# Performance work log

Measured on AMD Instinct MI355X. Metric: run time of the kernel, lower is better.

## Reference

```python
import jax, jax.numpy as jnp
import numpy as np

B, T, C = 2, 2048, 2048
H = 16
HD = C // H  # 128; kv_size == hidden_size so kv head dim == HD


def setup_inputs() -> dict:
    key = jax.random.key(0)
    ks = jax.random.split(key, 5)
    s = 0.02
    return {
        "x": jax.random.normal(ks[0], (B, T, C), dtype=jnp.float32),
        "Wq": jax.random.normal(ks[1], (C, C), dtype=jnp.float32) * s,
        "Wk": jax.random.normal(ks[2], (C, C), dtype=jnp.float32) * s,
        "Wv": jax.random.normal(ks[3], (C, C), dtype=jnp.float32) * s,
        "Wo": jax.random.normal(ks[4], (C, C), dtype=jnp.float32) * s,
    }


def reference(x, Wq, Wk, Wv, Wo):
    # Linear(bias=False): y = x @ W.T
    q = (x @ Wq.T).reshape(B, T, H, HD).transpose(0, 2, 1, 3)  # [B,H,T,HD]
    k = (x @ Wk.T).reshape(B, T, H, HD).transpose(0, 2, 1, 3)
    v = (x @ Wv.T).reshape(B, T, H, HD).transpose(0, 2, 1, 3)
    scale = 1.0 / np.sqrt(HD).astype(np.float32)
    att = jnp.einsum("bhqd,bhkd->bhqk", q, k) * scale  # [B,H,T,T]
    att = jax.nn.softmax(att, axis=-1)
    y = jnp.einsum("bhqk,bhkd->bhqd", att, v)  # [B,H,T,HD]
    y = y.transpose(0, 2, 1, 3).reshape(B, T, C)
    return y @ Wo.T
```

## Files before the change

kernel.cpp:

```cpp
#include <hip/hip_runtime.h>
#include <hip/hip_bf16.h>

typedef __attribute__((ext_vector_type(8))) short short8;
typedef __attribute__((ext_vector_type(4))) float f32x4;
typedef unsigned short u16;
typedef unsigned int u32;

__device__ __forceinline__ u16 f2bf(float f){
  __hip_bfloat16 h = __float2bfloat16(f);
  return *reinterpret_cast<u16*>(&h);
}

__device__ __forceinline__ void gld16(const void* g, void* l){
  __builtin_amdgcn_global_load_lds((const __attribute__((address_space(1))) void*)g,
                                   (__attribute__((address_space(3))) void*)l, 16, 0, 0);
}

#define SCHED0() __builtin_amdgcn_sched_barrier(0)

__global__ __launch_bounds__(256) void cvt_kernel(const float* __restrict__ src,
                                                  u16* __restrict__ dst, int n){
  int i0 = (blockIdx.x*256 + threadIdx.x)*4;
  int stride = gridDim.x*256*4;
  for (int i = i0; i < n; i += stride){
    float4 f = *reinterpret_cast<const float4*>(src + i);
    ushort4 u;
    u.x = f2bf(f.x); u.y = f2bf(f.y); u.z = f2bf(f.z); u.w = f2bf(f.w);
    *reinterpret_cast<ushort4*>(dst + i) = u;
  }
}

__device__ __forceinline__ void gemm256_body(const u16* __restrict__ A,
    const u16* __restrict__ W, void* __restrict__ outp, float scale, int epi)
{
  __shared__ alignas(16) u16 Lds[2*24576];
  const int tid = threadIdx.x;
  const int w = tid>>6, l = tid&63;
  const int l15 = l&15, lg = l>>4;
  const int wm = w>>1, wn = w&1;
  const int row0 = blockIdx.y*256, col0 = blockIdx.x*128;
  constexpr int K = 2048;
  constexpr int NT = K/64;

  f32x4 acc[4][4];
  #pragma unroll
  for (int i=0;i<4;i++)
    #pragma unroll
    for (int j=0;j<4;j++)
      #pragma unroll
      for (int r=0;r<4;r++) acc[i][j][r] = 0.f;

  int arow[2], acol[2], brow[2], bcol[2];
  #pragma unroll
  for (int p=0;p<2;p++){
    int s = p*512 + tid;
    arow[p] = s>>2;  acol[p] = ((s&3) ^ (arow[p]&3))*8;
    brow[p] = s>>3;  bcol[p] = ((s&7) ^ (brow[p]&7))*8;
  }

  auto stageB = [&](int buf, int kt){
    #pragma unroll
    for (int p=0;p<2;p++)
      gld16(W + (size_t)(col0 + brow[p])*K + kt*64 + bcol[p],
            &Lds[buf*24576 + 16384 + (p*512 + w*64)*8]);
  };
  auto stageA = [&](int buf, int kt, int kh){
    #pragma unroll
    for (int p=0;p<2;p++)
      gld16(A + (size_t)(row0 + arow[p])*K + kt*64 + kh*32 + acol[p],
            &Lds[buf*24576 + kh*8192 + (p*512 + w*64)*8]);
  };
  auto readA = [&](int buf, int ks, short8* af){
    #pragma unroll
    for (int i=0;i<4;i++){
      int r = wm*64 + i*16 + l15;
      int byt = buf*49152 + ks*16384 + r*64 + ((lg ^ (r&3))<<4);
      af[i] = *reinterpret_cast<const short8*>((const char*)Lds + byt);
    }
  };
  auto readB = [&](int buf, int ks, short8* bf){
    #pragma unroll
    for (int j=0;j<4;j++){
      int r = wn*64 + j*16 + l15;
      int byt = buf*49152 + 32768 + r*128 + ((((ks<<2)|lg) ^ (r&7))<<4);
      bf[j] = *reinterpret_cast<const short8*>((const char*)Lds + byt);
    }
  };

  stageB(0, 0); stageA(0, 0, 0); stageA(0, 0, 1);
  SCHED0();
  asm volatile("s_waitcnt vmcnt(2)" ::: "memory");
  __builtin_amdgcn_s_barrier();
  SCHED0();

  int cur = 0;
  for (int t=0; t<NT; ++t){
    int nxt = (t+1) & (NT-1);
    int nbuf = cur^1;
    short8 af[4], bf[4];
    stageB(nbuf, nxt);
    stageA(nbuf, nxt, 0);
    readA(cur, 0, af); readB(cur, 0, bf);
    asm volatile("s_waitcnt lgkmcnt(0)" ::: "memory");
    SCHED0();
    __builtin_amdgcn_s_setprio(1);
    #pragma unroll
    for (int i=0;i<4;i++)
      #pragma unroll
      for (int j=0;j<4;j++)
        acc[i][j] = __builtin_amdgcn_mfma_f32_16x16x32_bf16(af[i], bf[j], acc[i][j], 0, 0, 0);
    __builtin_amdgcn_s_setprio(0);
    SCHED0();
    asm volatile("s_waitcnt vmcnt(4)" ::: "memory");
    __builtin_amdgcn_s_barrier();
    SCHED0();
    stageA(nbuf, nxt, 1);
    readA(cur, 1, af); readB(cur, 1, bf);
    asm volatile("s_waitcnt lgkmcnt(0)" ::: "memory");
    SCHED0();
    __builtin_amdgcn_s_setprio(1);
    #pragma unroll
    for (int i=0;i<4;i++)
      #pragma unroll
      for (int j=0;j<4;j++)
        acc[i][j] = __builtin_amdgcn_mfma_f32_16x16x32_bf16(af[i], bf[j], acc[i][j], 0, 0, 0);
    __builtin_amdgcn_s_setprio(0);
    SCHED0();
    asm volatile("s_waitcnt vmcnt(2)" ::: "memory");
    __builtin_amdgcn_s_barrier();
    SCHED0();
    cur ^= 1;
  }

  if (epi == 0){
    u16* O = (u16*)outp;
    #pragma unroll
    for (int i=0;i<4;i++)
      #pragma unroll
      for (int j=0;j<4;j++)
        #pragma unroll
        for (int r=0;r<4;r++){
          int m = row0 + wm*64 + i*16 + lg*4 + r;
          int n = col0 + wn*64 + j*16 + l15;
          int b = m >> 11, tt = m & 2047;
          int h = n >> 7,  d = n & 127;
          O[(((size_t)(b*16 + h)*2048 + tt)<<7) + d] = f2bf(acc[i][j][r] * scale);
        }
  } else if (epi == 2){
    u16* O = (u16*)outp;
    #pragma unroll
    for (int i=0;i<4;i++)
      #pragma unroll
      for (int j=0;j<4;j++){
        int m0 = row0 + wm*64 + i*16 + lg*4;
        int n  = col0 + wn*64 + j*16 + l15;
        int b = m0 >> 11, tt = m0 & 2047;
        int h = n >> 7,  d = n & 127;
        ushort4 u;
        u.x = f2bf(acc[i][j][0]); u.y = f2bf(acc[i][j][1]);
        u.z = f2bf(acc[i][j][2]); u.w = f2bf(acc[i][j][3]);
        *reinterpret_cast<ushort4*>(&O[(((size_t)(b*16 + h)<<7) + d)*2048 + tt]) = u;
      }
  } else {
    float* O = (float*)outp;
    #pragma unroll
    for (int i=0;i<4;i++)
      #pragma unroll
      for (int j=0;j<4;j++)
        #pragma unroll
        for (int r=0;r<4;r++){
          int m = row0 + wm*64 + i*16 + lg*4 + r;
          int n = col0 + wn*64 + j*16 + l15;
          O[(size_t)m*2048 + n] = acc[i][j][r];
        }
  }
}

__global__ __launch_bounds__(512,2) void gemm_qkv(const u16* __restrict__ A,
    const u16* __restrict__ Wq, const u16* __restrict__ Wk, const u16* __restrict__ Wv,
    u16* __restrict__ qo, u16* __restrict__ ko, u16* __restrict__ vt, float qscale)
{
  const u16* W; void* O; float sc; int epi;
  if (blockIdx.z == 0){ W = Wq; O = qo; sc = qscale; epi = 0; }
  else if (blockIdx.z == 1){ W = Wk; O = ko; sc = 1.f; epi = 0; }
  else { W = Wv; O = vt; sc = 1.f; epi = 2; }
  gemm256_body(A, W, O, sc, epi);
}

__global__ __launch_bounds__(512,2) void gemm_out(const u16* __restrict__ A,
    const u16* __restrict__ W, float* __restrict__ O)
{
  gemm256_body(A, W, O, 1.f, 1);
}

__global__ __launch_bounds__(256,2) void attn_kernel(
    const u16* __restrict__ Q, const u16* __restrict__ Kg,
    const u16* __restrict__ Vt, u16* __restrict__ Y)
{
  __shared__ alignas(16) u16 Ks[2][64*128];
  __shared__ alignas(16) u16 Vs[2][128*64];
  const int tid = threadIdx.x;
  const int w = tid>>6, l = tid&63;
  const int l15 = l&15, lg = l>>4;

  int wg = blockIdx.x;
  int swz = (wg&7)*64 + (wg>>3);
  const int bh = swz >> 4;
  const int q0 = (swz & 15) * 128;

  short8 qf[2][4];
  #pragma unroll
  for (int mq=0;mq<2;mq++)
    #pragma unroll
    for (int ks=0;ks<4;ks++){
      int qrow = q0 + w*32 + mq*16 + l15;
      qf[mq][ks] = *reinterpret_cast<const short8*>(
          Q + ((size_t)bh*2048 + qrow)*128 + ks*32 + lg*8);
    }

  f32x4 accO[2][8];
  #pragma unroll
  for (int mq=0;mq<2;mq++)
    #pragma unroll
    for (int nd=0;nd<8;nd++)
      #pragma unroll
      for (int r=0;r<4;r++) accO[mq][nd][r] = 0.f;
  float mrun[2] = {-1e30f, -1e30f};
  float lrun[2] = {0.f, 0.f};

  int krow_[4], koff_[4], drow_[4], doff_[4];
  #pragma unroll
  for (int p=0;p<4;p++){
    int slot = p*256 + tid;
    int kr = slot>>4;
    int kb = (slot&15)*16;
    krow_[p] = kr; koff_[p] = (kb ^ ((kr&7)<<4)) >> 1;
    int dr = slot>>3;
    int db = (slot&7)*16;
    drow_[p] = dr; doff_[p] = (db ^ ((dr&7)<<4)) >> 1;
  }

  auto stage = [&](int buf, int kvt){
    int kv0 = kvt*64;
    #pragma unroll
    for (int p=0;p<4;p++){
      const u16* gk = Kg + ((size_t)bh*2048 + kv0 + krow_[p])*128 + koff_[p];
      gld16(gk, &Ks[buf][(size_t)(p*256 + w*64)*8]);
    }
    #pragma unroll
    for (int p=0;p<4;p++){
      const u16* gv = Vt + ((size_t)bh*128 + drow_[p])*2048 + kv0 + doff_[p];
      gld16(gv, &Vs[buf][(size_t)(p*256 + w*64)*8]);
    }
  };

  stage(0, 0);
  __syncthreads();

  int cur = 0;
  for (int kvt=0; kvt<32; ++kvt){
    if (kvt+1 < 32) stage(cur^1, kvt+1);

    f32x4 accS[2][4];
    #pragma unroll
    for (int mq=0;mq<2;mq++)
      #pragma unroll
      for (int kf=0;kf<4;kf++)
        #pragma unroll
        for (int r=0;r<4;r++) accS[mq][kf][r] = 0.f;
    #pragma unroll
    for (int kf=0;kf<4;kf++){
      short8 kfr[4];
      #pragma unroll
      for (int ks=0;ks<4;ks++){
        int kr = kf*16 + l15;
        int byt = kr*256 + ((ks*64 + lg*16) ^ ((kr&7)<<4));
        kfr[ks] = *reinterpret_cast<const short8*>((const char*)(&Ks[cur][0]) + byt);
      }
      #pragma unroll
      for (int mq=0;mq<2;mq++)
        #pragma unroll
        for (int ks=0;ks<4;ks++)
          accS[mq][kf] = __builtin_amdgcn_mfma_f32_16x16x32_bf16(kfr[ks], qf[mq][ks], accS[mq][kf], 0, 0, 0);
    }

    short8 pa[2][2];
    #pragma unroll
    for (int mq=0;mq<2;mq++){
      float tm = accS[mq][0][0];
      #pragma unroll
      for (int kf=0;kf<4;kf++)
        #pragma unroll
        for (int r=0;r<4;r++) tm = fmaxf(tm, accS[mq][kf][r]);
      tm = fmaxf(tm, __shfl_xor(tm, 16, 64));
      tm = fmaxf(tm, __shfl_xor(tm, 32, 64));
      float mn = fmaxf(mrun[mq], tm);
      float c = __expf(mrun[mq] - mn);
      mrun[mq] = mn;

      float pv[4][4];
      float rs = 0.f;
      #pragma unroll
      for (int kf=0;kf<4;kf++)
        #pragma unroll
        for (int r=0;r<4;r++){
          float e = __expf(accS[mq][kf][r] - mn);
          pv[kf][r] = e;
          rs += e;
        }
      rs += __shfl_xor(rs, 16, 64);
      rs += __shfl_xor(rs, 32, 64);
      lrun[mq] = lrun[mq]*c + rs;

      float cb[4];
      #pragma unroll
      for (int r=0;r<4;r++) cb[r] = __shfl(c, lg*4 + r, 64);
      #pragma unroll
      for (int nd=0;nd<8;nd++)
        #pragma unroll
        for (int r=0;r<4;r++) accO[mq][nd][r] *= cb[r];

      int pklo[4], pkhi[4];
      #pragma unroll
      for (int kf=0;kf<4;kf++){
        pklo[kf] = (int)((u32)f2bf(pv[kf][0]) | ((u32)f2bf(pv[kf][1])<<16));
        pkhi[kf] = (int)((u32)f2bf(pv[kf][2]) | ((u32)f2bf(pv[kf][3])<<16));
      }
      int s0 = l15 + 32*(lg&1);
      int s1 = s0 + 16;
      int hi = lg>>1;
      #pragma unroll
      for (int kk=0;kk<2;kk++){
        int a0 = __shfl(pklo[2*kk],   s0, 64);
        int a1 = __shfl(pklo[2*kk+1], s0, 64);
        int b0 = __shfl(pkhi[2*kk],   s0, 64);
        int b1 = __shfl(pkhi[2*kk+1], s0, 64);
        int c0 = __shfl(pklo[2*kk],   s1, 64);
        int c1 = __shfl(pklo[2*kk+1], s1, 64);
        int d0 = __shfl(pkhi[2*kk],   s1, 64);
        int d1 = __shfl(pkhi[2*kk+1], s1, 64);
        int4 wv;
        wv.x = hi ? a1 : a0;
        wv.y = hi ? b1 : b0;
        wv.z = hi ? c1 : c0;
        wv.w = hi ? d1 : d0;
        pa[mq][kk] = *reinterpret_cast<short8*>(&wv);
      }
    }

    #pragma unroll
    for (int nd=0;nd<8;nd++){
      short8 vf[2];
      #pragma unroll
      for (int kk=0;kk<2;kk++){
        int dr = nd*16 + l15;
        int byt = dr*128 + ((kk*64 + lg*16) ^ ((dr&7)<<4));
        vf[kk] = *reinterpret_cast<const short8*>((const char*)(&Vs[cur][0]) + byt);
      }
      #pragma unroll
      for (int mq=0;mq<2;mq++)
        #pragma unroll
        for (int kk=0;kk<2;kk++)
          accO[mq][nd] = __builtin_amdgcn_mfma_f32_16x16x32_bf16(pa[mq][kk], vf[kk], accO[mq][nd], 0, 0, 0);
    }

    __syncthreads();
    cur ^= 1;
  }

  const int b = bh >> 4, h = bh & 15;
  #pragma unroll
  for (int mq=0;mq<2;mq++){
    float lb[4];
    #pragma unroll
    for (int r=0;r<4;r++) lb[r] = __shfl(lrun[mq], lg*4 + r, 64);
    #pragma unroll
    for (int nd=0;nd<8;nd++)
      #pragma unroll
      for (int r=0;r<4;r++){
        int t = q0 + w*32 + mq*16 + lg*4 + r;
        int d = nd*16 + l15;
        float ov = accO[mq][nd][r] / lb[r];
        Y[((size_t)b*2048 + t)*2048 + h*128 + d] = f2bf(ov);
      }
  }
}

extern "C" void kernel_launch(void* const* d_in, const int* in_sizes, int n_in,
                              void* d_out, int out_size, void* d_ws, size_t ws_size,
                              hipStream_t stream)
{
  const float* x  = (const float*)d_in[0];
  const float* Wq = (const float*)d_in[1];
  const float* Wk = (const float*)d_in[2];
  const float* Wv = (const float*)d_in[3];
  const float* Wo = (const float*)d_in[4];
  float* out = (float*)d_out;
  char* ws = (char*)d_ws;

  const size_t MB = 1024*1024;
  u16* xb  = (u16*)(ws);
  u16* wqb = (u16*)(ws + 16*MB);
  u16* wkb = (u16*)(ws + 24*MB);
  u16* wvb = (u16*)(ws + 32*MB);
  u16* wob = (u16*)(ws + 40*MB);
  u16* qb  = (u16*)(ws + 48*MB);
  u16* kb  = (u16*)(ws + 64*MB);
  u16* vtb = (u16*)(ws + 80*MB);
  u16* yb  = wqb;

  cvt_kernel<<<2048, 256, 0, stream>>>(x,  xb,  4096*2048);
  cvt_kernel<<<1024, 256, 0, stream>>>(Wq, wqb, 2048*2048);
  cvt_kernel<<<1024, 256, 0, stream>>>(Wk, wkb, 2048*2048);
  cvt_kernel<<<1024, 256, 0, stream>>>(Wv, wvb, 2048*2048);
  cvt_kernel<<<1024, 256, 0, stream>>>(Wo, wob, 2048*2048);

  const float qscale = 0.08838834764831845f;
  gemm_qkv<<<dim3(16,16,3), 512, 0, stream>>>(xb, wqb, wkb, wvb, qb, kb, vtb, qscale);
  attn_kernel<<<512, 256, 0, stream>>>(qb, kb, vtb, yb);
  gemm_out<<<dim3(16,16), 512, 0, stream>>>(yb, wob, out);
}
```

Baseline: 287.2 us.

## Rewrite attention inner loop with 32x32x16 MFMA and lazy softmax rescale

The attention kernel moves from 16x16x32 MFMA tiles to 32x32x16 tiles, so each wave handles one 32-row query block and each lane owns a single query row's max and sum. The K/V shared-memory swizzle is changed to a 16-way XOR pattern to fit the new fragment access, and the P shuffle into MFMA operand layout now uses xor-32 exchanges instead of eight generic shuffles. Rescaling of the running max and output accumulator is skipped unless some row's max grows by more than 8, which cuts exp and multiply work but lets the unnormalised exponentials reach up to e^8 before bf16 conversion. The intent is fewer MFMA issues, fewer cross-lane shuffles and less softmax ALU work per KV tile.

```diff
diff --git a/kernel.cpp b/kernel.cpp
--- a/kernel.cpp
+++ b/kernel.cpp
@@ -3,6 +3,7 @@
 
 typedef __attribute__((ext_vector_type(8))) short short8;
 typedef __attribute__((ext_vector_type(4))) float f32x4;
+typedef __attribute__((ext_vector_type(16))) float f32x16;
 typedef unsigned short u16;
 typedef unsigned int u32;
 
@@ -198,60 +199,47 @@
     const u16* __restrict__ Vt, u16* __restrict__ Y)
 {
   __shared__ alignas(16) u16 Ks[2][64*128];
-  __shared__ alignas(16) u16 Vs[2][128*64];
+  __shared__ alignas(16) u16 Vs[2][64*128];
   const int tid = threadIdx.x;
   const int w = tid>>6, l = tid&63;
-  const int l15 = l&15, lg = l>>4;
-
-  int wg = blockIdx.x;
-  int swz = (wg&7)*64 + (wg>>3);
-  const int bh = swz >> 4;
-  const int q0 = (swz & 15) * 128;
-
-  short8 qf[2][4];
-  #pragma unroll
-  for (int mq=0;mq<2;mq++)
-    #pragma unroll
-    for (int ks=0;ks<4;ks++){
-      int qrow = q0 + w*32 + mq*16 + l15;
-      qf[mq][ks] = *reinterpret_cast<const short8*>(
-          Q + ((size_t)bh*2048 + qrow)*128 + ks*32 + lg*8);
-    }
-
-  f32x4 accO[2][8];
-  #pragma unroll
-  for (int mq=0;mq<2;mq++)
-    #pragma unroll
-    for (int nd=0;nd<8;nd++)
-      #pragma unroll
-      for (int r=0;r<4;r++) accO[mq][nd][r] = 0.f;
-  float mrun[2] = {-1e30f, -1e30f};
-  float lrun[2] = {0.f, 0.f};
-
-  int krow_[4], koff_[4], drow_[4], doff_[4];
+  const int l31 = l&31, hi = l>>5;
+  const int bh_swz = ((blockIdx.x&7)*64 + (blockIdx.x>>3));
+  const int bh = bh_swz >> 4;
+  const int q0 = (bh_swz & 15) * 128;
+
+  short8 qf[8];
+  #pragma unroll
+  for (int ds=0; ds<8; ds++)
+    qf[ds] = *reinterpret_cast<const short8*>(
+        Q + ((size_t)bh*2048 + q0 + w*32 + l31)*128 + ds*16 + hi*8);
+
+  f32x16 accO[4];
+  #pragma unroll
+  for (int dt=0;dt<4;dt++)
+    #pragma unroll
+    for (int r=0;r<16;r++) accO[dt][r] = 0.f;
+  float mrun = -1e30f, lrun = 0.f;
+
+  int krow_[4], kcol_[4], vd_[4], vkv_[4];
   #pragma unroll
   for (int p=0;p<4;p++){
-    int slot = p*256 + tid;
-    int kr = slot>>4;
-    int kb = (slot&15)*16;
-    krow_[p] = kr; koff_[p] = (kb ^ ((kr&7)<<4)) >> 1;
-    int dr = slot>>3;
-    int db = (slot&7)*16;
-    drow_[p] = dr; doff_[p] = (db ^ ((dr&7)<<4)) >> 1;
+    int s = p*256 + tid;
+    int r = s>>4, c = s&15;
+    int cu = c ^ (r&15);
+    krow_[p] = r;  kcol_[p] = cu*8;
+    vd_[p] = r*2 + (cu>>3);  vkv_[p] = (cu&7)*8;
   }
 
   auto stage = [&](int buf, int kvt){
     int kv0 = kvt*64;
     #pragma unroll
-    for (int p=0;p<4;p++){
-      const u16* gk = Kg + ((size_t)bh*2048 + kv0 + krow_[p])*128 + koff_[p];
-      gld16(gk, &Ks[buf][(size_t)(p*256 + w*64)*8]);
-    }
-    #pragma unroll
-    for (int p=0;p<4;p++){
-      const u16* gv = Vt + ((size_t)bh*128 + drow_[p])*2048 + kv0 + doff_[p];
-      gld16(gv, &Vs[buf][(size_t)(p*256 + w*64)*8]);
-    }
+    for (int p=0;p<4;p++)
+      gld16(Kg + ((size_t)bh*2048 + kv0 + krow_[p])*128 + kcol_[p],
+            &Ks[buf][(size_t)(p*256 + w*64)*8]);
+    #pragma unroll
+    for (int p=0;p<4;p++)
+      gld16(Vt + ((size_t)bh*128 + vd_[p])*2048 + kv0 + vkv_[p],
+            &Vs[buf][(size_t)(p*256 + w*64)*8]);
   };
 
   stage(0, 0);
@@ -261,128 +249,104 @@
   for (int kvt=0; kvt<32; ++kvt){
     if (kvt+1 < 32) stage(cur^1, kvt+1);
 
-    f32x4 accS[2][4];
-    #pragma unroll
-    for (int mq=0;mq<2;mq++)
-      #pragma unroll
-      for (int kf=0;kf<4;kf++)
+    f32x16 accS[2];
+    #pragma unroll
+    for (int kt=0;kt<2;kt++)
+      #pragma unroll
+      for (int r=0;r<16;r++) accS[kt][r] = 0.f;
+    #pragma unroll
+    for (int kt=0;kt<2;kt++){
+      #pragma unroll
+      for (int ds=0;ds<8;ds++){
+        int row = kt*32 + l31;
+        int byt = row*256 + (((ds*2 + hi) ^ (row&15))<<4);
+        short8 kf = *reinterpret_cast<const short8*>((const char*)(&Ks[cur][0]) + byt);
+        accS[kt] = __builtin_amdgcn_mfma_f32_32x32x16_bf16(kf, qf[ds], accS[kt], 0, 0, 0);
+      }
+    }
+
+    float pmax = accS[0][0];
+    #pragma unroll
+    for (int kt=0;kt<2;kt++)
+      #pragma unroll
+      for (int r=0;r<16;r++) pmax = fmaxf(pmax, accS[kt][r]);
+    pmax = fmaxf(pmax, __shfl_xor(pmax, 32, 64));
+    if (__any(pmax > mrun + 8.f)){
+      float mn = fmaxf(mrun, pmax);
+      float c = __expf(mrun - mn);
+      mrun = mn;
+      lrun *= c;
+      #pragma unroll
+      for (int r=0;r<16;r++){
+        int qrow = (r&3) + 8*(r>>2) + 4*hi;
+        float cr = __shfl(c, qrow, 64);
         #pragma unroll
-        for (int r=0;r<4;r++) accS[mq][kf][r] = 0.f;
-    #pragma unroll
-    for (int kf=0;kf<4;kf++){
-      short8 kfr[4];
+        for (int dt=0;dt<4;dt++) accO[dt][r] *= cr;
+      }
+    }
+
+    float rs = 0.f;
+    short8 pa[4];
+    #pragma unroll
+    for (int kt=0;kt<2;kt++){
+      #pragma unroll
+      for (int b=0;b<2;b++){
+        float e0 = __expf(accS[kt][b*8+0] - mrun);
+        float e1 = __expf(accS[kt][b*8+1] - mrun);
+        float e2 = __expf(accS[kt][b*8+2] - mrun);
+        float e3 = __expf(accS[kt][b*8+3] - mrun);
+        float e4 = __expf(accS[kt][b*8+4] - mrun);
+        float e5 = __expf(accS[kt][b*8+5] - mrun);
+        float e6 = __expf(accS[kt][b*8+6] - mrun);
+        float e7 = __expf(accS[kt][b*8+7] - mrun);
+        rs += (e0+e1)+(e2+e3)+(e4+e5)+(e6+e7);
+        u32 x01 = (u32)f2bf(e0) | ((u32)f2bf(e1)<<16);
+        u32 x23 = (u32)f2bf(e2) | ((u32)f2bf(e3)<<16);
+        u32 y01 = (u32)f2bf(e4) | ((u32)f2bf(e5)<<16);
+        u32 y23 = (u32)f2bf(e6) | ((u32)f2bf(e7)<<16);
+        u32 sx_x01 = __shfl_xor(x01, 32, 64);
+        u32 sx_x23 = __shfl_xor(x23, 32, 64);
+        u32 sx_y01 = __shfl_xor(y01, 32, 64);
+        u32 sx_y23 = __shfl_xor(y23, 32, 64);
+        int4 wv;
+        wv.x = (int)(hi ? sx_y01 : x01);
+        wv.y = (int)(hi ? sx_y23 : x23);
+        wv.z = (int)(hi ? y01 : sx_x01);
+        wv.w = (int)(hi ? y23 : sx_x23);
+        pa[kt*2+b] = *reinterpret_cast<short8*>(&wv);
+      }
+    }
+    rs += __shfl_xor(rs, 32, 64);
+    lrun += rs;
+
+    #pragma unroll
+    for (int dt=0;dt<4;dt++){
       #pragma unroll
       for (int ks=0;ks<4;ks++){
-        int kr = kf*16 + l15;
-        int byt = kr*256 + ((ks*64 + lg*16) ^ ((kr&7)<<4));
-        kfr[ks] = *reinterpret_cast<const short8*>((const char*)(&Ks[cur][0]) + byt);
-      }
-      #pragma unroll
-      for (int mq=0;mq<2;mq++)
-        #pragma unroll
-        for (int ks=0;ks<4;ks++)
-          accS[mq][kf] = __builtin_amdgcn_mfma_f32_16x16x32_bf16(kfr[ks], qf[mq][ks], accS[mq][kf], 0, 0, 0);
-    }
-
-    short8 pa[2][2];
-    #pragma unroll
-    for (int mq=0;mq<2;mq++){
-      float tm = accS[mq][0][0];
-      #pragma unroll
-      for (int kf=0;kf<4;kf++)
-        #pragma unroll
-        for (int r=0;r<4;r++) tm = fmaxf(tm, accS[mq][kf][r]);
-      tm = fmaxf(tm, __shfl_xor(tm, 16, 64));
-      tm = fmaxf(tm, __shfl_xor(tm, 32, 64));
-      float mn = fmaxf(mrun[mq], tm);
-      float c = __expf(mrun[mq] - mn);
-      mrun[mq] = mn;
-
-      float pv[4][4];
-      float rs = 0.f;
-      #pragma unroll
-      for (int kf=0;kf<4;kf++)
-        #pragma unroll
-        for (int r=0;r<4;r++){
-          float e = __expf(accS[mq][kf][r] - mn);
-          pv[kf][r] = e;
-          rs += e;
-        }
-      rs += __shfl_xor(rs, 16, 64);
-      rs += __shfl_xor(rs, 32, 64);
-      lrun[mq] = lrun[mq]*c + rs;
-
-      float cb[4];
-      #pragma unroll
-      for (int r=0;r<4;r++) cb[r] = __shfl(c, lg*4 + r, 64);
-      #pragma unroll
-      for (int nd=0;nd<8;nd++)
-        #pragma unroll
-        for (int r=0;r<4;r++) accO[mq][nd][r] *= cb[r];
-
-      int pklo[4], pkhi[4];
-      #pragma unroll
-      for (int kf=0;kf<4;kf++){
-        pklo[kf] = (int)((u32)f2bf(pv[kf][0]) | ((u32)f2bf(pv[kf][1])<<16));
-        pkhi[kf] = (int)((u32)f2bf(pv[kf][2]) | ((u32)f2bf(pv[kf][3])<<16));
-      }
-      int s0 = l15 + 32*(lg&1);
-      int s1 = s0 + 16;
-      int hi = lg>>1;
-      #pragma unroll
-      for (int kk=0;kk<2;kk++){
-        int a0 = __shfl(pklo[2*kk],   s0, 64);
-        int a1 = __shfl(pklo[2*kk+1], s0, 64);
-        int b0 = __shfl(pkhi[2*kk],   s0, 64);
-        int b1 = __shfl(pkhi[2*kk+1], s0, 64);
-        int c0 = __shfl(pklo[2*kk],   s1, 64);
-        int c1 = __shfl(pklo[2*kk+1], s1, 64);
-        int d0 = __shfl(pkhi[2*kk],   s1, 64);
-        int d1 = __shfl(pkhi[2*kk+1], s1, 64);
-        int4 wv;
-        wv.x = hi ? a1 : a0;
-        wv.y = hi ? b1 : b0;
-        wv.z = hi ? c1 : c0;
-        wv.w = hi ? d1 : d0;
-        pa[mq][kk] = *reinterpret_cast<short8*>(&wv);
-      }
-    }
-
-    #pragma unroll
-    for (int nd=0;nd<8;nd++){
-      short8 vf[2];
-      #pragma unroll
-      for (int kk=0;kk<2;kk++){
-        int dr = nd*16 + l15;
-        int byt = dr*128 + ((kk*64 + lg*16) ^ ((dr&7)<<4));
-        vf[kk] = *reinterpret_cast<const short8*>((const char*)(&Vs[cur][0]) + byt);
-      }
-      #pragma unroll
-      for (int mq=0;mq<2;mq++)
-        #pragma unroll
-        for (int kk=0;kk<2;kk++)
-          accO[mq][nd] = __builtin_amdgcn_mfma_f32_16x16x32_bf16(pa[mq][kk], vf[kk], accO[mq][nd], 0, 0, 0);
+        int d = dt*32 + l31;
+        int cu = (d&1)*8 + ks*2 + hi;
+        int byt = (d>>1)*256 + ((cu ^ ((d>>1)&15))<<4);
+        short8 vf = *reinterpret_cast<const short8*>((const char*)(&Vs[cur][0]) + byt);
+        accO[dt] = __builtin_amdgcn_mfma_f32_32x32x16_bf16(pa[ks], vf, accO[dt], 0, 0, 0);
+      }
     }
 
     __syncthreads();
     cur ^= 1;
   }
 
-  const int b = bh >> 4, h = bh & 15;
-  #pragma unroll
-  for (int mq=0;mq<2;mq++){
-    float lb[4];
-    #pragma unroll
-    for (int r=0;r<4;r++) lb[r] = __shfl(lrun[mq], lg*4 + r, 64);
-    #pragma unroll
-    for (int nd=0;nd<8;nd++)
-      #pragma unroll
-      for (int r=0;r<4;r++){
-        int t = q0 + w*32 + mq*16 + lg*4 + r;
-        int d = nd*16 + l15;
-        float ov = accO[mq][nd][r] / lb[r];
-        Y[((size_t)b*2048 + t)*2048 + h*128 + d] = f2bf(ov);
-      }
+  const int b_ = bh >> 4, h_ = bh & 15;
+  float inv = 1.f / lrun;
+  #pragma unroll
+  for (int r=0;r<16;r++){
+    int qrow = (r&3) + 8*(r>>2) + 4*hi;
+    float lr = __shfl(inv, qrow, 64);
+    int t = q0 + w*32 + qrow;
+    #pragma unroll
+    for (int dt=0;dt<4;dt++){
+      int d = dt*32 + l31;
+      Y[((size_t)b_*2048 + t)*2048 + h_*128 + d] = f2bf(accO[dt][r] * lr);
+    }
   }
 }
 
```

Result: faster. 266.8 us (-7.1%).
